# Optimization experiments

Hardware: AMD Instinct MI355X
Metric: run time of the kernel (lower is better)

The kernel has to match this reference:

```python
import jax, jax.numpy as jnp
import numpy as np

B, S, HID = 2, 2048, 2048
H = 16
NOPE, ROPE, V_DIM, KV_RANK = 128, 64, 128, 512
Q_DIM = NOPE + ROPE  # 192
EPS = 1e-6
NEG = -1e9


def setup_inputs() -> dict:
    key = jax.random.key(0)
    ks = jax.random.split(key, 5)
    return {
        "hidden_states": jax.random.normal(ks[0], (B, S, HID), jnp.float32),
        "q_proj_w": jax.random.normal(ks[1], (H * Q_DIM, HID), jnp.float32) * (HID ** -0.5),
        "kv_a_proj_w": jax.random.normal(ks[2], (KV_RANK + ROPE, HID), jnp.float32) * (HID ** -0.5),
        "kv_a_ln_w": jnp.ones((KV_RANK,), jnp.float32),
        "kv_b_proj_w": jax.random.normal(ks[3], (H * (NOPE + V_DIM), KV_RANK), jnp.float32) * (KV_RANK ** -0.5),
        "o_proj_w": jax.random.normal(ks[4], (HID, H * V_DIM), jnp.float32) * ((H * V_DIM) ** -0.5),
    }


def _rmsnorm(x, w):
    xf = x.astype(jnp.float32)
    var = jnp.mean(xf * xf, axis=-1, keepdims=True)
    return (w * (xf * jax.lax.rsqrt(var + EPS)).astype(x.dtype))


def reference(hidden_states, q_proj_w, kv_a_proj_w, kv_a_ln_w, kv_b_proj_w, o_proj_w):
    b, s, _ = hidden_states.shape
    scaling = Q_DIM ** -0.5

    # query projection -> [b, h, s, q_dim]
    q = (hidden_states @ q_proj_w.T).reshape(b, s, H, Q_DIM).transpose(0, 2, 1, 3)

    # latent kv projection
    compressed = hidden_states @ kv_a_proj_w.T            # [b, s, kv_rank+rope]
    k_pass_lat = compressed[..., :KV_RANK]                # [b, s, kv_rank]
    k_rot = compressed[..., KV_RANK:]                     # [b, s, rope]

    kv = (_rmsnorm(k_pass_lat, kv_a_ln_w) @ kv_b_proj_w.T)  # [b, s, h*(nope+v)]
    kv = kv.reshape(b, s, H, NOPE + V_DIM).transpose(0, 2, 1, 3)  # [b, h, s, nope+v]
    k_pass = kv[..., :NOPE]                               # [b, h, s, nope]
    v = kv[..., NOPE:]                                    # [b, h, s, v]

    k_rot = jnp.broadcast_to(k_rot[:, None, :, :], (b, H, s, ROPE))
    k = jnp.concatenate([k_pass, k_rot], axis=-1)         # [b, h, s, q_dim]

    # causal attention (eager path), softmax in fp32
    scores = jnp.einsum("bhqd,bhkd->bhqk", q, k) * scaling
    causal = jnp.tril(jnp.ones((s, s), bool))
    scores = jnp.where(causal[None, None], scores, NEG)
    probs = jax.nn.softmax(scores.astype(jnp.float32), axis=-1).astype(q.dtype)

    out = jnp.einsum("bhqk,bhkd->bhqd", probs, v)         # [b, h, s, v]
    out = out.transpose(0, 2, 1, 3).reshape(b, s, H * V_DIM)
    return out @ o_proj_w.T
```

## Files before the change

### kernel.cpp

```cpp
#include <hip/hip_runtime.h>
#include <stdint.h>
#include <stddef.h>

#define B_    2
#define S_    2048
#define HID_  2048
#define H_    16
#define NOPE_ 128
#define ROPE_ 64
#define VD_   128
#define RANK_ 512
#define QD_   192
#define M_    4096
#define NEGV  (-1e9f)

typedef __attribute__((ext_vector_type(8))) __bf16 bf16x8;
typedef __attribute__((ext_vector_type(8))) short  short8;
typedef __attribute__((ext_vector_type(4))) short  short4v;
typedef __attribute__((ext_vector_type(4))) float  f32x4;

__device__ __forceinline__ short f2bf(float f) {
  uint32_t u = __builtin_bit_cast(uint32_t, f);
  u += 0x7fffu + ((u >> 16) & 1u);
  return (short)(u >> 16);
}

__device__ __forceinline__ void gll16(const void* g, void* l) {
  __builtin_amdgcn_global_load_lds(
      (__attribute__((address_space(1))) void*)(g),
      (__attribute__((address_space(3))) void*)(l), 16, 0, 0);
}

__device__ __forceinline__ f32x4 mfma16(short8 a, short8 b, f32x4 c) {
  return __builtin_amdgcn_mfma_f32_16x16x32_bf16(
      __builtin_bit_cast(bf16x8, a), __builtin_bit_cast(bf16x8, b), c, 0, 0, 0);
}

__global__ void k_cast4(const float* __restrict__ in, short* __restrict__ out, int n4) {
  int i = blockIdx.x * blockDim.x + threadIdx.x;
  if (i >= n4) return;
  float4 v = *(const float4*)(in + (size_t)i * 4);
  short4v o = { f2bf(v.x), f2bf(v.y), f2bf(v.z), f2bf(v.w) };
  *(short4v*)(out + (size_t)i * 4) = o;
}

__global__ void k_cast_kva(const float* __restrict__ in, short* __restrict__ out) {
  int i = blockIdx.x * blockDim.x + threadIdx.x;
  int e = i * 4;
  int r = e >> 11, c = e & 2047;
  short4v o = {0, 0, 0, 0};
  if (r < 576) {
    float4 v = *(const float4*)(in + (size_t)r * 2048 + c);
    o[0] = f2bf(v.x); o[1] = f2bf(v.y); o[2] = f2bf(v.z); o[3] = f2bf(v.w);
  }
  *(short4v*)(out + e) = o;
}

template <typename OutT>
__global__ __launch_bounds__(256) void k_gemm_bt(
    const short* __restrict__ A, const short* __restrict__ Bm,
    OutT* __restrict__ C, int M, int N, int K)
{
  __shared__ __align__(16) short As[128 * 64];
  __shared__ __align__(16) short Bs[128 * 64];
  const int tid = threadIdx.x;
  const int lane = tid & 63, wid = tid >> 6;
  const int l15 = lane & 15, lhi = lane >> 4;
  const int brow = blockIdx.y * 128, bcol = blockIdx.x * 128;
  const int wr = (wid >> 1) * 64, wc = (wid & 1) * 64;

  f32x4 acc[4][4];
#pragma unroll
  for (int i = 0; i < 4; ++i)
#pragma unroll
    for (int j = 0; j < 4; ++j) acc[i][j] = (f32x4)0.f;

  const int srow = lane >> 3;
  const int scol = ((lane & 7) ^ srow) * 8;

  for (int k0 = 0; k0 < K; k0 += 64) {
    __syncthreads();
#pragma unroll
    for (int i = 0; i < 4; ++i) {
      int seg = wid * 4 + i;
      int row = seg * 8 + srow;
      gll16(A  + (size_t)(brow + row) * K + k0 + scol, &As[seg * 512]);
      gll16(Bm + (size_t)(bcol + row) * K + k0 + scol, &Bs[seg * 512]);
    }
    __syncthreads();
#pragma unroll
    for (int ks = 0; ks < 2; ++ks) {
      short8 af[4], bfr[4];
#pragma unroll
      for (int i = 0; i < 4; ++i) {
        int r = wr + i * 16 + l15;
        af[i] = *(const short8*)&As[r * 64 + (((ks * 4 + lhi) ^ (l15 & 7)) << 3)];
      }
#pragma unroll
      for (int j = 0; j < 4; ++j) {
        int r = wc + j * 16 + l15;
        bfr[j] = *(const short8*)&Bs[r * 64 + (((ks * 4 + lhi) ^ (l15 & 7)) << 3)];
      }
#pragma unroll
      for (int i = 0; i < 4; ++i)
#pragma unroll
        for (int j = 0; j < 4; ++j) acc[i][j] = mfma16(af[i], bfr[j], acc[i][j]);
    }
  }
#pragma unroll
  for (int i = 0; i < 4; ++i) {
    int r0 = brow + wr + i * 16 + lhi * 4;
#pragma unroll
    for (int j = 0; j < 4; ++j) {
      int c = bcol + wc + j * 16 + l15;
#pragma unroll
      for (int t = 0; t < 4; ++t) {
        float v = acc[i][j][t];
        if constexpr (__is_same(OutT, float)) C[(size_t)(r0 + t) * N + c] = v;
        else                                  C[(size_t)(r0 + t) * N + c] = f2bf(v);
      }
    }
  }
}

__global__ __launch_bounds__(256) void k_rms(
    const float* __restrict__ comp,
    const float* __restrict__ w,
    short* __restrict__ normed,
    short* __restrict__ krot)
{
  __shared__ float red[4];
  const int row = blockIdx.x, tid = threadIdx.x;
  const float* x = comp + (size_t)row * 640;
  float v0 = x[tid], v1 = x[tid + 256];
  float ss = v0 * v0 + v1 * v1;
#pragma unroll
  for (int off = 1; off < 64; off <<= 1) ss += __shfl_xor(ss, off);
  if ((tid & 63) == 0) red[tid >> 6] = ss;
  __syncthreads();
  float rs = rsqrtf((red[0] + red[1] + red[2] + red[3]) * (1.f / 512.f) + 1e-6f);
  normed[(size_t)row * 512 + tid]       = f2bf(w[tid] * v0 * rs);
  normed[(size_t)row * 512 + tid + 256] = f2bf(w[tid + 256] * v1 * rs);
  if (tid < 64) krot[(size_t)row * 64 + tid] = f2bf(x[512 + tid]);
}

__global__ __launch_bounds__(256) void k_vtrans(
    const short* __restrict__ kv, short* __restrict__ vt)
{
  __shared__ __align__(16) short t[64][136];
  const int tid = threadIdx.x;
  const int st = blockIdx.x, bh = blockIdx.y;
  const int b = bh >> 4, h = bh & 15;
  const int s0 = st * 64;
#pragma unroll
  for (int i = 0; i < 4; ++i) {
    int e8 = i * 256 + tid;
    int r = e8 >> 4, c = (e8 & 15) * 8;
    short8 v = *(const short8*)&kv[(size_t)(b * S_ + s0 + r) * 4096 + h * 256 + 128 + c];
    *(short8*)&t[r][c] = v;
  }
  __syncthreads();
#pragma unroll
  for (int i = 0; i < 4; ++i) {
    int e8 = i * 256 + tid;
    int d = e8 >> 3, sc = (e8 & 7) * 8;
    short8 o;
#pragma unroll
    for (int k = 0; k < 8; ++k) o[k] = t[sc + k][d];
    *(short8*)&vt[((size_t)bh * 128 + d) * S_ + s0 + sc] = o;
  }
}

__global__ __launch_bounds__(256) void k_attn(
    const short* __restrict__ q,
    const short* __restrict__ kv,
    const short* __restrict__ krot,
    const short* __restrict__ vt,
    short* __restrict__ outp)
{
  __shared__ __align__(16) short Kp[64 * 128];
  __shared__ __align__(16) short Kr[64 * 64];
  __shared__ __align__(16) short Vt[128 * 64];
  __shared__ __align__(16) short Ps[64 * 64];

  const int tid = threadIdx.x, lane = tid & 63, wid = tid >> 6;
  const int l15 = lane & 15, lhi = lane >> 4;
  const int qt = blockIdx.x, bh = blockIdx.y;
  const int b = bh >> 4, h = bh & 15;
  const int q0 = qt * 64;

  short8 qf[6];
  {
    const short* qp = q + (size_t)(b * S_ + q0 + wid * 16 + l15) * (H_ * QD_) + h * QD_ + lhi * 8;
#pragma unroll
    for (int ks = 0; ks < 6; ++ks) qf[ks] = *(const short8*)(qp + ks * 32);
  }

  float m_run[4] = {-1e30f, -1e30f, -1e30f, -1e30f};
  float l_run[4] = {0.f, 0.f, 0.f, 0.f};
  f32x4 oa[8];
#pragma unroll
  for (int j = 0; j < 8; ++j) oa[j] = (f32x4)0.f;

  const int sr8 = lane >> 3;
  const int sc8 = ((lane & 7) ^ sr8) * 8;
  const float scale = 0.07216878f;

  for (int kt = 0; kt <= qt; ++kt) {
    const int krow0 = b * S_ + kt * 64;
    __syncthreads();
#pragma unroll
    for (int i = 0; i < 4; ++i) {
      int seg = wid * 4 + i;
      int row = seg * 4 + (lane >> 4);
      int col = ((lane & 15) ^ (row & 7)) * 8;
      gll16(kv + (size_t)(krow0 + row) * 4096 + h * 256 + col, &Kp[seg * 512]);
    }
#pragma unroll
    for (int i = 0; i < 2; ++i) {
      int seg = wid * 2 + i;
      int row = seg * 8 + sr8;
      gll16(krot + (size_t)(krow0 + row) * 64 + sc8, &Kr[seg * 512]);
    }
#pragma unroll
    for (int i = 0; i < 4; ++i) {
      int seg = wid * 4 + i;
      int d = seg * 8 + sr8;
      gll16(vt + ((size_t)bh * 128 + d) * S_ + kt * 64 + sc8, &Vt[seg * 512]);
    }
    __syncthreads();

    f32x4 sf[4];
#pragma unroll
    for (int fc = 0; fc < 4; ++fc) sf[fc] = (f32x4)0.f;
#pragma unroll
    for (int fc = 0; fc < 4; ++fc) {
      int n = fc * 16 + l15, nx = n & 7;
#pragma unroll
      for (int ks = 0; ks < 4; ++ks) {
        short8 kf = *(const short8*)&Kp[n * 128 + (((ks * 4 + lhi) ^ nx) << 3)];
        sf[fc] = mfma16(qf[ks], kf, sf[fc]);
      }
#pragma unroll
      for (int ks = 4; ks < 6; ++ks) {
        short8 kf = *(const short8*)&Kr[n * 64 + ((((ks - 4) * 4 + lhi) ^ nx) << 3)];
        sf[fc] = mfma16(qf[ks], kf, sf[fc]);
      }
    }
    if (kt == qt) {
#pragma unroll
      for (int fc = 0; fc < 4; ++fc) {
        int kl = fc * 16 + l15;
#pragma unroll
        for (int r = 0; r < 4; ++r) {
          int ql = wid * 16 + lhi * 4 + r;
          sf[fc][r] = (kl <= ql) ? sf[fc][r] * scale : NEGV;
        }
      }
    } else {
#pragma unroll
      for (int fc = 0; fc < 4; ++fc)
#pragma unroll
        for (int r = 0; r < 4; ++r) sf[fc][r] *= scale;
    }
    float mnew[4], scf[4], rsum[4];
#pragma unroll
    for (int r = 0; r < 4; ++r) {
      float t = fmaxf(fmaxf(sf[0][r], sf[1][r]), fmaxf(sf[2][r], sf[3][r]));
#pragma unroll
      for (int off = 1; off < 16; off <<= 1) t = fmaxf(t, __shfl_xor(t, off));
      mnew[r] = fmaxf(m_run[r], t);
      scf[r] = __expf(m_run[r] - mnew[r]);
      m_run[r] = mnew[r];
      rsum[r] = 0.f;
    }
#pragma unroll
    for (int fc = 0; fc < 4; ++fc)
#pragma unroll
      for (int r = 0; r < 4; ++r) {
        float p = __expf(sf[fc][r] - mnew[r]);
        sf[fc][r] = p;
        rsum[r] += p;
      }
#pragma unroll
    for (int r = 0; r < 4; ++r) {
      float t = rsum[r];
#pragma unroll
      for (int off = 1; off < 16; off <<= 1) t += __shfl_xor(t, off);
      l_run[r] = l_run[r] * scf[r] + t;
    }
#pragma unroll
    for (int j = 0; j < 8; ++j)
#pragma unroll
      for (int r = 0; r < 4; ++r) oa[j][r] *= scf[r];
#pragma unroll
    for (int fc = 0; fc < 4; ++fc)
#pragma unroll
      for (int r = 0; r < 4; ++r) {
        int pr = wid * 16 + lhi * 4 + r;
        int pc = fc * 16 + l15;
        Ps[pr * 64 + ((((pc >> 3) ^ (pr & 7)) << 3) | (pc & 7))] = f2bf(sf[fc][r]);
      }
    __syncthreads();
    short8 pa[2];
    {
      int prow = wid * 16 + l15, px = prow & 7;
#pragma unroll
      for (int ks = 0; ks < 2; ++ks)
        pa[ks] = *(const short8*)&Ps[prow * 64 + (((ks * 4 + lhi) ^ px) << 3)];
    }
#pragma unroll
    for (int j = 0; j < 8; ++j) {
      int d = j * 16 + l15, dx = d & 7;
#pragma unroll
      for (int ks = 0; ks < 2; ++ks) {
        short8 vb = *(const short8*)&Vt[d * 64 + (((ks * 4 + lhi) ^ dx) << 3)];
        oa[j] = mfma16(pa[ks], vb, oa[j]);
      }
    }
  }
#pragma unroll
  for (int j = 0; j < 8; ++j)
#pragma unroll
    for (int r = 0; r < 4; ++r) {
      size_t row = (size_t)(b * S_ + q0 + wid * 16 + lhi * 4 + r);
      int col = h * 128 + j * 16 + l15;
      outp[row * 2048 + col] = f2bf(oa[j][r] / l_run[r]);
    }
}

extern "C" void kernel_launch(void* const* d_in, const int* in_sizes, int n_in,
                              void* d_out, int out_size, void* d_ws, size_t ws_size,
                              hipStream_t stream) {
  const float* hidden = (const float*)d_in[0];
  const float* qw     = (const float*)d_in[1];
  const float* kvaw   = (const float*)d_in[2];
  const float* lnw    = (const float*)d_in[3];
  const float* kvbw   = (const float*)d_in[4];
  const float* ow     = (const float*)d_in[5];

  char* ws = (char*)d_ws;
  short* hidb  = (short*)(ws + 0);
  short* qwb   = (short*)(ws + 16777216);
  short* kvawb = (short*)(ws + 29360128);
  short* kvbwb = (short*)(ws + 31981568);
  short* owb   = (short*)(ws + 36175872);
  short* qb    = (short*)(ws + 44564480);
  float* comp  = (float*)(ws + 69730304);
  short* normb = (short*)(ws + 80216064);
  short* krotb = (short*)(ws + 84410368);
  short* kvb   = (short*)(ws + 84934656);
  short* vtb   = (short*)(ws + 118489088);
  short* attnb = (short*)(ws + 135266304);

  k_cast4<<<8192, 256, 0, stream>>>(hidden, hidb, 2097152);
  k_cast4<<<6144, 256, 0, stream>>>(qw, qwb, 1572864);
  k_cast_kva<<<1280, 256, 0, stream>>>(kvaw, kvawb);
  k_cast4<<<2048, 256, 0, stream>>>(kvbw, kvbwb, 524288);
  k_cast4<<<4096, 256, 0, stream>>>(ow, owb, 1048576);

  k_gemm_bt<short><<<dim3(24, 32), 256, 0, stream>>>(hidb, qwb, qb, M_, 3072, 2048);
  k_gemm_bt<float><<<dim3(5, 32), 256, 0, stream>>>(hidb, kvawb, comp, M_, 640, 2048);
  k_rms<<<4096, 256, 0, stream>>>(comp, lnw, normb, krotb);
  k_gemm_bt<short><<<dim3(32, 32), 256, 0, stream>>>(normb, kvbwb, kvb, M_, 4096, 512);
  k_vtrans<<<dim3(32, 32), 256, 0, stream>>>(kvb, vtb);

  k_attn<<<dim3(32, 32), 256, 0, stream>>>(qb, kvb, krotb, vtb, attnb);

  k_gemm_bt<float><<<dim3(16, 32), 256, 0, stream>>>(attnb, owb, (float*)d_out, M_, 2048, 2048);
}
```

Before: 537.3 us.

## Double-buffer K/V tiles in attention and schedule heavy query tiles first

The attention kernel now keeps two LDS buffers for the K-nope, K-rope and V^T tiles. It prefetches tile kt+1 with global-to-LDS loads while computing tile kt, so load latency overlaps the MFMA work. Query tiles are launched in reverse order, so blocks with the longest causal loops start first and the tail of the grid is shorter. The barrier before the P·V step now waits only on LDS traffic, so the prefetch can stay in flight. In exchange, LDS use per block roughly doubles, to about 88KB, which may lower occupancy.

```diff
diff --git a/kernel.cpp b/kernel.cpp
--- a/kernel.cpp
+++ b/kernel.cpp
@@ -178,57 +178,72 @@
     const short* __restrict__ vt,
     short* __restrict__ outp)
 {
-  __shared__ __align__(16) short Kp[64 * 128];
-  __shared__ __align__(16) short Kr[64 * 64];
-  __shared__ __align__(16) short Vt[128 * 64];
+  __shared__ __align__(16) short Kp0[64 * 128], Kp1[64 * 128];
+  __shared__ __align__(16) short Kr0[64 * 64],  Kr1[64 * 64];
+  __shared__ __align__(16) short Vt0[128 * 64], Vt1[128 * 64];
   __shared__ __align__(16) short Ps[64 * 64];
 
   const int tid = threadIdx.x, lane = tid & 63, wid = tid >> 6;
   const int l15 = lane & 15, lhi = lane >> 4;
-  const int qt = blockIdx.x, bh = blockIdx.y;
+  const int qt = (int)gridDim.x - 1 - (int)blockIdx.x;
+  const int bh = blockIdx.y;
   const int b = bh >> 4, h = bh & 15;
   const int q0 = qt * 64;
 
-  short8 qf[6];
-  {
-    const short* qp = q + (size_t)(b * S_ + q0 + wid * 16 + l15) * (H_ * QD_) + h * QD_ + lhi * 8;
-#pragma unroll
-    for (int ks = 0; ks < 6; ++ks) qf[ks] = *(const short8*)(qp + ks * 32);
-  }
-
-  float m_run[4] = {-1e30f, -1e30f, -1e30f, -1e30f};
-  float l_run[4] = {0.f, 0.f, 0.f, 0.f};
-  f32x4 oa[8];
-#pragma unroll
-  for (int j = 0; j < 8; ++j) oa[j] = (f32x4)0.f;
-
   const int sr8 = lane >> 3;
   const int sc8 = ((lane & 7) ^ sr8) * 8;
-  const float scale = 0.07216878f;
-
-  for (int kt = 0; kt <= qt; ++kt) {
+
+  auto STAGE = [&](int sel, int kt) {
+    short* KpS = sel ? Kp1 : Kp0;
+    short* KrS = sel ? Kr1 : Kr0;
+    short* VtS = sel ? Vt1 : Vt0;
     const int krow0 = b * S_ + kt * 64;
-    __syncthreads();
 #pragma unroll
     for (int i = 0; i < 4; ++i) {
       int seg = wid * 4 + i;
       int row = seg * 4 + (lane >> 4);
       int col = ((lane & 15) ^ (row & 7)) * 8;
-      gll16(kv + (size_t)(krow0 + row) * 4096 + h * 256 + col, &Kp[seg * 512]);
+      gll16(kv + (size_t)(krow0 + row) * 4096 + h * 256 + col, &KpS[seg * 512]);
     }
 #pragma unroll
     for (int i = 0; i < 2; ++i) {
       int seg = wid * 2 + i;
       int row = seg * 8 + sr8;
-      gll16(krot + (size_t)(krow0 + row) * 64 + sc8, &Kr[seg * 512]);
+      gll16(krot + (size_t)(krow0 + row) * 64 + sc8, &KrS[seg * 512]);
     }
 #pragma unroll
     for (int i = 0; i < 4; ++i) {
       int seg = wid * 4 + i;
       int d = seg * 8 + sr8;
-      gll16(vt + ((size_t)bh * 128 + d) * S_ + kt * 64 + sc8, &Vt[seg * 512]);
-    }
+      gll16(vt + ((size_t)bh * 128 + d) * S_ + kt * 64 + sc8, &VtS[seg * 512]);
+    }
+  };
+
+  short8 qf[6];
+  {
+    const short* qp = q + (size_t)(b * S_ + q0 + wid * 16 + l15) * (H_ * QD_) + h * QD_ + lhi * 8;
+#pragma unroll
+    for (int ks = 0; ks < 6; ++ks) qf[ks] = *(const short8*)(qp + ks * 32);
+  }
+
+  float m_run[4] = {-1e30f, -1e30f, -1e30f, -1e30f};
+  float l_run[4] = {0.f, 0.f, 0.f, 0.f};
+  f32x4 oa[8];
+#pragma unroll
+  for (int j = 0; j < 8; ++j) oa[j] = (f32x4)0.f;
+
+  const float scale = 0.07216878f;
+
+  STAGE(0, 0);
+
+  for (int kt = 0; kt <= qt; ++kt) {
+    const int cur = kt & 1;
     __syncthreads();
+    if (kt < qt) STAGE(cur ^ 1, kt + 1);
+
+    const short* KpS = cur ? Kp1 : Kp0;
+    const short* KrS = cur ? Kr1 : Kr0;
+    const short* VtS = cur ? Vt1 : Vt0;
 
     f32x4 sf[4];
 #pragma unroll
@@ -238,12 +253,12 @@
       int n = fc * 16 + l15, nx = n & 7;
 #pragma unroll
       for (int ks = 0; ks < 4; ++ks) {
-        short8 kf = *(const short8*)&Kp[n * 128 + (((ks * 4 + lhi) ^ nx) << 3)];
+        short8 kf = *(const short8*)&KpS[n * 128 + (((ks * 4 + lhi) ^ nx) << 3)];
         sf[fc] = mfma16(qf[ks], kf, sf[fc]);
       }
 #pragma unroll
       for (int ks = 4; ks < 6; ++ks) {
-        short8 kf = *(const short8*)&Kr[n * 64 + ((((ks - 4) * 4 + lhi) ^ nx) << 3)];
+        short8 kf = *(const short8*)&KrS[n * 64 + ((((ks - 4) * 4 + lhi) ^ nx) << 3)];
         sf[fc] = mfma16(qf[ks], kf, sf[fc]);
       }
     }
@@ -301,7 +316,8 @@
         int pc = fc * 16 + l15;
         Ps[pr * 64 + ((((pc >> 3) ^ (pr & 7)) << 3) | (pc & 7))] = f2bf(sf[fc][r]);
       }
-    __syncthreads();
+    asm volatile("s_waitcnt lgkmcnt(0)" ::: "memory");
+    __builtin_amdgcn_s_barrier();
     short8 pa[2];
     {
       int prow = wid * 16 + l15, px = prow & 7;
@@ -314,7 +330,7 @@
       int d = j * 16 + l15, dx = d & 7;
 #pragma unroll
       for (int ks = 0; ks < 2; ++ks) {
-        short8 vb = *(const short8*)&Vt[d * 64 + (((ks * 4 + lhi) ^ dx) << 3)];
+        short8 vb = *(const short8*)&VtS[d * 64 + (((ks * 4 + lhi) ^ dx) << 3)];
         oa[j] = mfma16(pa[ks], vb, oa[j]);
       }
     }
```

Measured after the change: 613.2 us. +14.1%, slower.
